# Kernel tuning notes

Measured on AMD Instinct MI355X. Metric: run time of the kernel, lower is better.

The kernel has to match this reference:

```python
import jax, jax.numpy as jnp
import numpy as np

N = 131072   # n_nodes == n_edges (required by the broadcast in the original module)
C = 256      # node_channels == edge_channels (required by the broadcast)
EPS_BN = 1e-5
EPS = 1e-5


def _linear_params(key, out_c, in_c):
    k1, k2 = jax.random.split(key)
    bound = 1.0 / np.sqrt(in_c)
    W = jax.random.uniform(k1, (out_c, in_c), minval=-bound, maxval=bound, dtype=jnp.float32)
    b = jax.random.uniform(k2, (out_c,), minval=-bound, maxval=bound, dtype=jnp.float32)
    return W, b


def setup_inputs() -> dict:
    key = jax.random.key(0)
    ks = jax.random.split(key, 10)
    h = jax.random.normal(ks[0], (N, C), dtype=jnp.float32)
    e = jax.random.normal(ks[1], (N, C), dtype=jnp.float32)
    edge_index = jax.random.randint(ks[2], (2, N), 0, N, dtype=jnp.int64)
    A_w, A_b = _linear_params(ks[3], C, C)
    B_w, B_b = _linear_params(ks[4], C, C)
    C_w, C_b = _linear_params(ks[5], C, C)
    D_w, D_b = _linear_params(ks[6], C, C)
    U_w, U_b = _linear_params(ks[7], C, C)
    V_w, V_b = _linear_params(ks[8], C, C)
    bn_gamma = jnp.ones((C,), dtype=jnp.float32)
    bn_beta = jnp.zeros((C,), dtype=jnp.float32)
    return dict(h=h, edge_index=edge_index, e=e,
                A_w=A_w, A_b=A_b, B_w=B_w, B_b=B_b,
                C_w=C_w, C_b=C_b, D_w=D_w, D_b=D_b,
                bn_gamma=bn_gamma, bn_beta=bn_beta,
                U_w=U_w, U_b=U_b, V_w=V_w, V_b=V_b)


def reference(h, edge_index, e,
              A_w, A_b, B_w, B_b, C_w, C_b, D_w, D_b,
              bn_gamma, bn_beta, U_w, U_b, V_w, V_b):
    row, col = edge_index[0], edge_index[1]
    # gather + four parallel linears, summed: [E, C]
    e_out = (h[row] @ A_w.T + A_b
             + h[col] @ B_w.T + B_b
             + e[col] @ C_w.T + C_b
             + e[row] @ D_w.T + D_b)
    # BatchNorm1d (training mode: batch stats, biased variance) + ReLU
    mu = jnp.mean(e_out, axis=0)
    var = jnp.var(e_out, axis=0)
    e_out = jax.nn.relu(bn_gamma * (e_out - mu) * jax.lax.rsqrt(var + EPS_BN) + bn_beta)
    # scatter-add edge messages into node-indexed e, then sigmoid-normalize over dim 0
    e_new = e.at[row].add(e_out)
    e_new = jax.nn.sigmoid(e_new)
    e_new = e_new / (jnp.sum(e_new, axis=0, keepdims=True) + EPS)
    # final gather-multiply-reduce: (e_new * V(h[col])).sum(0) broadcasts [N,C]*[E,C] with N==E
    h_out = h @ U_w.T + U_b + jnp.sum(e_new * (h[col] @ V_w.T + V_b), axis=0)
    h_out = jax.nn.relu(h_out)
    return h_out, e_new
```

## Files before the change

kernel.cpp:

```cpp
#include <hip/hip_runtime.h>
#include <hip/hip_bf16.h>


typedef __attribute__((ext_vector_type(8))) short bf16x8;
typedef __attribute__((ext_vector_type(4))) float f32x4;

__device__ __forceinline__ float b2f(unsigned int lo16) {
  union { unsigned int u; float f; } c; c.u = lo16 << 16; return c.f;
}
__device__ __forceinline__ float lof(unsigned int u) { return b2f(u & 0xffffu); }
__device__ __forceinline__ float hif(unsigned int u) { return b2f(u >> 16); }
__device__ __forceinline__ unsigned int f2b(float f) {
  union { float f; unsigned int u; } c; c.f = f;
  unsigned int u = c.u;
  u += 0x7fffu + ((u >> 16) & 1u);
  return u >> 16;
}

__device__ __forceinline__ void prep_chunk(const float* __restrict__ src,
                                           unsigned short* __restrict__ dst, int g) {
  int mtile = g >> 9;
  int rem = g & 511;
  int r = rem >> 5, k8 = rem & 31;
  const float4* s = reinterpret_cast<const float4*>(src + (((size_t)mtile * 16 + r) << 8) + k8 * 8);
  float4 v0 = s[0], v1 = s[1];
  uint4 o;
  o.x = f2b(v0.x) | (f2b(v0.y) << 16);
  o.y = f2b(v0.z) | (f2b(v0.w) << 16);
  o.z = f2b(v1.x) | (f2b(v1.y) << 16);
  o.w = f2b(v1.z) | (f2b(v1.w) << 16);
  *reinterpret_cast<uint4*>(dst + ((size_t)mtile * 512 + k8 * 16 + r) * 8) = o;
}

__global__ __launch_bounds__(256) void prep_he(const float* __restrict__ h,
                                               unsigned short* __restrict__ h_t,
                                               const float* __restrict__ e,
                                               unsigned short* __restrict__ e_t,
                                               int nChunksEach) {
  int g = blockIdx.x * 256 + threadIdx.x;
  if (g < nChunksEach) prep_chunk(h, h_t, g);
  else if (g < 2 * nChunksEach) prep_chunk(e, e_t, g - nChunksEach);
}

__global__ __launch_bounds__(256) void prep_weights(
    const float* __restrict__ s0, const float* __restrict__ s1,
    const float* __restrict__ s2, const float* __restrict__ s3,
    const float* __restrict__ s4, const float* __restrict__ s5,
    unsigned short* __restrict__ W1h, unsigned short* __restrict__ W1e,
    unsigned short* __restrict__ W2t,
    const float* __restrict__ Ab, const float* __restrict__ Db,
    const float* __restrict__ Bb, const float* __restrict__ Cb,
    const float* __restrict__ Vb, const float* __restrict__ Ub,
    float* __restrict__ b1, float* __restrict__ b2,
    float* __restrict__ sums, float* __restrict__ sumsq,
    float* __restrict__ colsum, float* __restrict__ Traw,
    const int* __restrict__ ei, int* __restrict__ mode) {
  int g = blockIdx.x * 256 + threadIdx.x;
  if (blockIdx.x == 0) {
    const int t = threadIdx.x;
    b1[t] = Ab[t] + Db[t];
    b1[256 + t] = Bb[t] + Cb[t];
    b2[t] = Vb[t];
    b2[256 + t] = Ub[t];
    sums[t] = 0.f; sumsq[t] = 0.f; colsum[t] = 0.f; Traw[t] = 0.f;
    if (t == 0) {
      int m = 0;
#pragma unroll
      for (int i = 1; i < 64; i += 2) m |= ei[i];
      *mode = (m == 0) ? 1 : 0;
    }
  }
  int sel = g >> 13;
  int gg = g & 8191;
  const float* src; unsigned short* dst;
  switch (sel) {
    case 0: src = s0; dst = W1h; break;
    case 1: src = s1; dst = W1h + 65536; break;
    case 2: src = s2; dst = W1e; break;
    case 3: src = s3; dst = W1e + 65536; break;
    case 4: src = s4; dst = W2t; break;
    default: src = s5; dst = W2t + 65536; break;
  }
  prep_chunk(src, dst, gg);
}

__global__ __launch_bounds__(256) void gemm_bt2(
    const unsigned short* __restrict__ Ah, const unsigned short* __restrict__ Ae,
    const unsigned short* __restrict__ Bh, const unsigned short* __restrict__ Be,
    const float* __restrict__ bias, unsigned short* __restrict__ Cmat,
    int O, int nColBlk, int ktSteps, int nBlk) {
  __shared__ char lds[49152];
  const int cpx = nBlk >> 3;
  const int hw = blockIdx.x;
  const int bid = (hw % 8) * cpx + hw / 8;
  const int colBlk = bid % nColBlk;
  const int rowBlk = bid / nColBlk;
  const int tid = threadIdx.x;
  const int w = tid >> 6, lane = tid & 63;
  const int wm = w >> 1, wn = w & 1;

  const size_t aTileOff = (size_t)(rowBlk * 8 + w * 2) * 8192 + lane * 16;
  const size_t bTileOff = (size_t)(colBlk * 8 + w * 2) * 8192 + lane * 16;
  const int wOff0 = (w * 2) * 1024;
  const int wOff1 = (w * 2 + 1) * 1024;

  f32x4 acc[4][4] = {};

  auto stage = [&](int kt, char* bufA, char* bufB) {
    const char* Ab_ = (const char*)(kt < 8 ? Ah : Ae) + aTileOff + (size_t)(kt & 7) * 1024;
    const char* Bb_ = (const char*)(kt < 8 ? Bh : Be) + bTileOff + (size_t)(kt & 7) * 1024;
    __builtin_amdgcn_global_load_lds((const __attribute__((address_space(1))) void*)Ab_,
                                     (__attribute__((address_space(3))) void*)(bufA + wOff0), 16, 0, 0);
    __builtin_amdgcn_global_load_lds((const __attribute__((address_space(1))) void*)(Ab_ + 8192),
                                     (__attribute__((address_space(3))) void*)(bufA + wOff1), 16, 0, 0);
    __builtin_amdgcn_global_load_lds((const __attribute__((address_space(1))) void*)Bb_,
                                     (__attribute__((address_space(3))) void*)(bufB + wOff0), 16, 0, 0);
    __builtin_amdgcn_global_load_lds((const __attribute__((address_space(1))) void*)(Bb_ + 8192),
                                     (__attribute__((address_space(3))) void*)(bufB + wOff1), 16, 0, 0);
  };
  auto computeFrom = [&](const char* bufA, const char* bufB) {
    bf16x8 a[4], b[4];
#pragma unroll
    for (int mi = 0; mi < 4; ++mi)
      a[mi] = *reinterpret_cast<const bf16x8*>(bufA + (wm * 4 + mi) * 1024 + lane * 16);
#pragma unroll
    for (int ni = 0; ni < 4; ++ni)
      b[ni] = *reinterpret_cast<const bf16x8*>(bufB + (wn * 4 + ni) * 1024 + lane * 16);
#pragma unroll
    for (int mi = 0; mi < 4; ++mi)
#pragma unroll
      for (int ni = 0; ni < 4; ++ni)
        acc[mi][ni] = __builtin_amdgcn_mfma_f32_16x16x32_bf16(a[mi], b[ni], acc[mi][ni], 0, 0, 0);
  };

  char* A0 = lds;          char* A1 = lds + 8192;   char* A2 = lds + 16384;
  char* B0 = lds + 24576;  char* B1 = lds + 32768;  char* B2 = lds + 40960;

  stage(0, A0, B0);
  stage(1, A1, B1);
  char *Ac = A0, *An = A1, *Aq = A2;
  char *Bc = B0, *Bn = B1, *Bq = B2;

#pragma unroll 1
  for (int kt = 0; kt < ktSteps; ++kt) {
    if (kt + 1 < ktSteps) {
      asm volatile("s_waitcnt vmcnt(4)" ::: "memory");
    } else {
      asm volatile("s_waitcnt vmcnt(0)" ::: "memory");
    }
    __builtin_amdgcn_s_barrier();
    asm volatile("" ::: "memory");
    __builtin_amdgcn_sched_barrier(0);
    if (kt + 2 < ktSteps) stage(kt + 2, Aq, Bq);
    computeFrom(Ac, Bc);
    char* tA = Ac; Ac = An; An = Aq; Aq = tA;
    char* tB = Bc; Bc = Bn; Bn = Bq; Bq = tB;
  }

  const int rb = rowBlk * 128 + wm * 64 + ((lane >> 4) << 2);
  const int cb = colBlk * 128 + wn * 64 + (lane & 15);
#pragma unroll
  for (int mi = 0; mi < 4; ++mi) {
#pragma unroll
    for (int ni = 0; ni < 4; ++ni) {
      const int coln = cb + ni * 16;
      const float bz = bias[coln];
      const size_t base = (size_t)(rb + mi * 16) * O + coln;
#pragma unroll
      for (int r = 0; r < 4; ++r)
        Cmat[base + (size_t)r * O] = (unsigned short)f2b(acc[mi][ni][r] + bz);
    }
  }
}

__global__ __launch_bounds__(256) void edge_stats(
    const unsigned short* __restrict__ PRPC,
    const int* __restrict__ rows_s, const int* __restrict__ cols_s,
    float* __restrict__ sums, float* __restrict__ sumsq) {
  __shared__ float red[8][256];
  const int c8 = threadIdx.x & 31;
  const int sub = threadIdx.x >> 5;
  float s[8], q[8];
#pragma unroll
  for (int j = 0; j < 8; ++j) { s[j] = 0.f; q[j] = 0.f; }
#pragma unroll 1
  for (int grp = 0; grp < 2; ++grp) {
    const int kb = blockIdx.x * 64 + grp * 32 + sub * 4;
    int r[4], cj[4];
#pragma unroll
    for (int u = 0; u < 4; ++u) { r[u] = rows_s[kb + u]; cj[u] = cols_s[kb + u]; }
    uint4 pr[4], pc[4];
#pragma unroll
    for (int u = 0; u < 4; ++u)
      pr[u] = *reinterpret_cast<const uint4*>(PRPC + (size_t)r[u] * 512 + c8 * 8);
#pragma unroll
    for (int u = 0; u < 4; ++u)
      pc[u] = *reinterpret_cast<const uint4*>(PRPC + (size_t)cj[u] * 512 + 256 + c8 * 8);
#pragma unroll
    for (int u = 0; u < 4; ++u) {
      const unsigned int rw[4] = {pr[u].x, pr[u].y, pr[u].z, pr[u].w};
      const unsigned int cw[4] = {pc[u].x, pc[u].y, pc[u].z, pc[u].w};
#pragma unroll
      for (int p4 = 0; p4 < 4; ++p4) {
        const float v0 = lof(rw[p4]) + lof(cw[p4]);
        const float v1 = hif(rw[p4]) + hif(cw[p4]);
        s[2 * p4] += v0;     q[2 * p4] += v0 * v0;
        s[2 * p4 + 1] += v1; q[2 * p4 + 1] += v1 * v1;
      }
    }
  }
#pragma unroll
  for (int j = 0; j < 8; ++j) red[sub][c8 * 8 + j] = s[j];
  __syncthreads();
  {
    const int c = threadIdx.x;
    float t = 0.f;
#pragma unroll
    for (int u2 = 0; u2 < 8; ++u2) t += red[u2][c];
    atomicAdd(sums + c, t);
  }
  __syncthreads();
#pragma unroll
  for (int j = 0; j < 8; ++j) red[sub][c8 * 8 + j] = q[j];
  __syncthreads();
  {
    const int c = threadIdx.x;
    float t = 0.f;
#pragma unroll
    for (int u2 = 0; u2 < 8; ++u2) t += red[u2][c];
    atomicAdd(sumsq + c, t);
  }
}

__global__ __launch_bounds__(256) void hist_rows(const int* __restrict__ ei,
                                                 const int* __restrict__ modep,
                                                 int* __restrict__ cnt, int Nn) {
  const int k = blockIdx.x * 256 + threadIdx.x;
  if (k >= Nn) return;
  const int row = (*modep) ? ei[2 * k] : ei[k];
  atomicAdd(&cnt[row], 1);
}

__global__ __launch_bounds__(256) void scan1(const int* __restrict__ cnt,
                                             int* __restrict__ bsum) {
  __shared__ int red[256];
  const int t = threadIdx.x;
  red[t] = cnt[blockIdx.x * 256 + t];
  __syncthreads();
#pragma unroll
  for (int s = 128; s > 0; s >>= 1) {
    if (t < s) red[t] += red[t + s];
    __syncthreads();
  }
  if (t == 0) bsum[blockIdx.x] = red[0];
}

__global__ __launch_bounds__(512) void scan2(int* __restrict__ bsum, int nb) {
  __shared__ int tmp[512];
  const int t = threadIdx.x;
  const int own = (t < nb) ? bsum[t] : 0;
  tmp[t] = own;
  __syncthreads();
  for (int off = 1; off < 512; off <<= 1) {
    int v = (t >= off) ? tmp[t - off] : 0;
    __syncthreads();
    tmp[t] += v;
    __syncthreads();
  }
  if (t < nb) bsum[t] = tmp[t] - own;
}

__global__ __launch_bounds__(256) void scan3(const int* __restrict__ cnt,
                                             const int* __restrict__ bsum,
                                             int* __restrict__ base, int Nn) {
  __shared__ int tmp[256];
  const int t = threadIdx.x;
  const int gid = blockIdx.x * 256 + t;
  const int own = cnt[gid];
  tmp[t] = own;
  __syncthreads();
  for (int off = 1; off < 256; off <<= 1) {
    int v = (t >= off) ? tmp[t - off] : 0;
    __syncthreads();
    tmp[t] += v;
    __syncthreads();
  }
  base[gid] = tmp[t] - own + bsum[blockIdx.x];
  if (gid == 0) base[Nn] = Nn;
}

__global__ __launch_bounds__(256) void scatter_eids(const int* __restrict__ ei,
                                                    const int* __restrict__ modep,
                                                    const int* __restrict__ base,
                                                    int* __restrict__ cnt,
                                                    int* __restrict__ rows_s,
                                                    int* __restrict__ cols_s, int Nn) {
  const int k = blockIdx.x * 256 + threadIdx.x;
  if (k >= Nn) return;
  int row, col;
  if (*modep) { row = ei[2 * k]; col = ei[2 * (Nn + k)]; }
  else        { row = ei[k];     col = ei[Nn + k]; }
  const int pos = base[row] + atomicAdd(&cnt[row], -1) - 1;
  rows_s[pos] = row;
  cols_s[pos] = col;
}

#define GCAP 1024
__global__ __launch_bounds__(256) void gather_sig_T(
    const float* __restrict__ e, const unsigned short* __restrict__ PRPC,
    const int* __restrict__ base, const int* __restrict__ cols_s,
    const int* __restrict__ ei, const int* __restrict__ modep,
    const unsigned short* __restrict__ VU,
    const float* __restrict__ sums, const float* __restrict__ sumsq,
    const float* __restrict__ gamma, const float* __restrict__ beta,
    unsigned short* __restrict__ accB, float* __restrict__ colsum,
    float* __restrict__ Traw, float invE, int Nn) {
  __shared__ float red[4][256];
  __shared__ int colsL[GCAP];
  __shared__ int baseL[65];
  const int lane = threadIdx.x & 63, w = threadIdx.x >> 6;
  const int n0 = blockIdx.x * 64;
  if (threadIdx.x < 65) baseL[threadIdx.x] = base[n0 + threadIdx.x];
  __syncthreads();
  const int bstart = baseL[0];
  const int bcount = baseL[64] - bstart;
  for (int qq = threadIdx.x; qq < bcount && qq < GCAP; qq += 256)
    colsL[qq] = cols_s[bstart + qq];
  const float4 sm = *reinterpret_cast<const float4*>(sums + lane * 4);
  const float4 sq = *reinterpret_cast<const float4*>(sumsq + lane * 4);
  const float4 gm = *reinterpret_cast<const float4*>(gamma + lane * 4);
  const float4 bt = *reinterpret_cast<const float4*>(beta + lane * 4);
  float4 sc, sh;
  {
    const float mx = sm.x * invE, my = sm.y * invE, mz = sm.z * invE, mw = sm.w * invE;
    sc.x = gm.x * rsqrtf(fmaxf(sq.x * invE - mx * mx, 0.f) + 1e-5f);
    sc.y = gm.y * rsqrtf(fmaxf(sq.y * invE - my * my, 0.f) + 1e-5f);
    sc.z = gm.z * rsqrtf(fmaxf(sq.z * invE - mz * mz, 0.f) + 1e-5f);
    sc.w = gm.w * rsqrtf(fmaxf(sq.w * invE - mw * mw, 0.f) + 1e-5f);
    sh.x = bt.x - mx * sc.x; sh.y = bt.y - my * sc.y;
    sh.z = bt.z - mz * sc.z; sh.w = bt.w - mw * sc.w;
  }
  __syncthreads();
  const int mode = *modep;
  float s0 = 0.f, s1 = 0.f, s2 = 0.f, s3 = 0.f;
  float t0 = 0.f, t1 = 0.f, t2 = 0.f, t3 = 0.f;
  const int i0 = n0 + w * 16;
  int p = baseL[w * 16];
  const int pendW = baseL[w * 16 + 16];
  uint2 pcn; pcn.x = 0; pcn.y = 0;
  if (p < pendW) {
    const int q0 = p - bstart;
    const int cj = (q0 < GCAP) ? colsL[q0] : cols_s[p];
    pcn = *reinterpret_cast<const uint2*>(PRPC + (size_t)cj * 512 + 256 + lane * 4);
  }
  float4 ev = *reinterpret_cast<const float4*>(e + (size_t)i0 * 256 + lane * 4);
  uint2 prv = *reinterpret_cast<const uint2*>(PRPC + (size_t)i0 * 512 + lane * 4);
#pragma unroll 1
  for (int it = 0; it < 16; ++it) {
    const int i = i0 + it;
    const int colT = mode ? ei[2 * (Nn + i)] : ei[Nn + i];
    const uint2 hv = *reinterpret_cast<const uint2*>(VU + (size_t)colT * 512 + lane * 4);
    float4 v = ev;
    const uint2 pr = prv;
    if (it + 1 < 16) {
      ev = *reinterpret_cast<const float4*>(e + (size_t)(i + 1) * 256 + lane * 4);
      prv = *reinterpret_cast<const uint2*>(PRPC + (size_t)(i + 1) * 512 + lane * 4);
    }
    const float pr0 = lof(pr.x), pr1 = hif(pr.x), pr2 = lof(pr.y), pr3 = hif(pr.y);
    const int pe = baseL[w * 16 + it + 1];
#pragma unroll 1
    while (p < pe) {
      const uint2 pc = pcn;
      if (p + 1 < pendW) {
        const int qn = p + 1 - bstart;
        const int cj = (qn < GCAP) ? colsL[qn] : cols_s[p + 1];
        pcn = *reinterpret_cast<const uint2*>(PRPC + (size_t)cj * 512 + 256 + lane * 4);
      }
      v.x += fmaxf(fmaf(sc.x, pr0 + lof(pc.x), sh.x), 0.f);
      v.y += fmaxf(fmaf(sc.y, pr1 + hif(pc.x), sh.y), 0.f);
      v.z += fmaxf(fmaf(sc.z, pr2 + lof(pc.y), sh.z), 0.f);
      v.w += fmaxf(fmaf(sc.w, pr3 + hif(pc.y), sh.w), 0.f);
      ++p;
    }
    v.x = 1.f / (1.f + __expf(-v.x));
    v.y = 1.f / (1.f + __expf(-v.y));
    v.z = 1.f / (1.f + __expf(-v.z));
    v.w = 1.f / (1.f + __expf(-v.w));
    uint2 ob;
    ob.x = f2b(v.x) | (f2b(v.y) << 16);
    ob.y = f2b(v.z) | (f2b(v.w) << 16);
    *reinterpret_cast<uint2*>(accB + (size_t)i * 256 + lane * 4) = ob;
    s0 += v.x; s1 += v.y; s2 += v.z; s3 += v.w;
    t0 += v.x * lof(hv.x); t1 += v.y * hif(hv.x);
    t2 += v.z * lof(hv.y); t3 += v.w * hif(hv.y);
  }
  red[w][lane * 4 + 0] = s0;
  red[w][lane * 4 + 1] = s1;
  red[w][lane * 4 + 2] = s2;
  red[w][lane * 4 + 3] = s3;
  __syncthreads();
  {
    const int c = threadIdx.x;
    atomicAdd(colsum + c, red[0][c] + red[1][c] + red[2][c] + red[3][c]);
  }
  __syncthreads();
  red[w][lane * 4 + 0] = t0;
  red[w][lane * 4 + 1] = t1;
  red[w][lane * 4 + 2] = t2;
  red[w][lane * 4 + 3] = t3;
  __syncthreads();
  {
    const int c = threadIdx.x;
    atomicAdd(Traw + c, red[0][c] + red[1][c] + red[2][c] + red[3][c]);
  }
}

__global__ __launch_bounds__(256) void finalize(
    const unsigned short* __restrict__ accB, const unsigned short* __restrict__ VU,
    const float* __restrict__ colsum, const float* __restrict__ Traw,
    float* __restrict__ outE, float* __restrict__ outH, int nChunks) {
  const int g = blockIdx.x * 256 + threadIdx.x;
  if (g >= nChunks) return;
  const int i = g >> 5, c8 = g & 31;
  const float4 cs0 = *reinterpret_cast<const float4*>(colsum + c8 * 8);
  const float4 cs1 = *reinterpret_cast<const float4*>(colsum + c8 * 8 + 4);
  const float4 tr0 = *reinterpret_cast<const float4*>(Traw + c8 * 8);
  const float4 tr1 = *reinterpret_cast<const float4*>(Traw + c8 * 8 + 4);
  float iv[8] = {1.f / (cs0.x + 1e-5f), 1.f / (cs0.y + 1e-5f),
                 1.f / (cs0.z + 1e-5f), 1.f / (cs0.w + 1e-5f),
                 1.f / (cs1.x + 1e-5f), 1.f / (cs1.y + 1e-5f),
                 1.f / (cs1.z + 1e-5f), 1.f / (cs1.w + 1e-5f)};
  float tt[8] = {tr0.x * iv[0], tr0.y * iv[1], tr0.z * iv[2], tr0.w * iv[3],
                 tr1.x * iv[4], tr1.y * iv[5], tr1.z * iv[6], tr1.w * iv[7]};
  const uint4 sb = *reinterpret_cast<const uint4*>(accB + (size_t)i * 256 + c8 * 8);
  const unsigned int sw[4] = {sb.x, sb.y, sb.z, sb.w};
  float4 e0, e1;
  e0.x = lof(sw[0]) * iv[0]; e0.y = hif(sw[0]) * iv[1];
  e0.z = lof(sw[1]) * iv[2]; e0.w = hif(sw[1]) * iv[3];
  e1.x = lof(sw[2]) * iv[4]; e1.y = hif(sw[2]) * iv[5];
  e1.z = lof(sw[3]) * iv[6]; e1.w = hif(sw[3]) * iv[7];
  float4* qe = reinterpret_cast<float4*>(outE + (size_t)i * 256 + c8 * 8);
  qe[0] = e0; qe[1] = e1;
  const uint4 hu = *reinterpret_cast<const uint4*>(VU + (size_t)i * 512 + 256 + c8 * 8);
  float4 o0, o1;
  o0.x = fmaxf(lof(hu.x) + tt[0], 0.f);
  o0.y = fmaxf(hif(hu.x) + tt[1], 0.f);
  o0.z = fmaxf(lof(hu.y) + tt[2], 0.f);
  o0.w = fmaxf(hif(hu.y) + tt[3], 0.f);
  o1.x = fmaxf(lof(hu.z) + tt[4], 0.f);
  o1.y = fmaxf(hif(hu.z) + tt[5], 0.f);
  o1.z = fmaxf(lof(hu.w) + tt[6], 0.f);
  o1.w = fmaxf(hif(hu.w) + tt[7], 0.f);
  float4* qh = reinterpret_cast<float4*>(outH + (size_t)i * 256 + c8 * 8);
  qh[0] = o0; qh[1] = o1;
}

extern "C" void kernel_launch(void* const* d_in, const int* in_sizes, int n_in,
                              void* d_out, int out_size, void* d_ws, size_t ws_size,
                              hipStream_t stream) {
  const float* h     = (const float*)d_in[0];
  const int*   ei    = (const int*)d_in[1];
  const float* e     = (const float*)d_in[2];
  const float* Aw    = (const float*)d_in[3];
  const float* Ab    = (const float*)d_in[4];
  const float* Bw    = (const float*)d_in[5];
  const float* Bb    = (const float*)d_in[6];
  const float* Cw    = (const float*)d_in[7];
  const float* Cb    = (const float*)d_in[8];
  const float* Dw    = (const float*)d_in[9];
  const float* Db    = (const float*)d_in[10];
  const float* gamma = (const float*)d_in[11];
  const float* beta  = (const float*)d_in[12];
  const float* Uw    = (const float*)d_in[13];
  const float* Ub    = (const float*)d_in[14];
  const float* Vw    = (const float*)d_in[15];
  const float* Vb    = (const float*)d_in[16];
  const int N = in_sizes[0] / 256;

  char* ws = (char*)d_ws;
  unsigned short* W1h = (unsigned short*)(ws + 0x0);
  unsigned short* W1e = (unsigned short*)(ws + 0x40000);
  unsigned short* W2t = (unsigned short*)(ws + 0x80000);
  float* b1     = (float*)(ws + 0xC0000);
  float* b2     = (float*)(ws + 0xC0800);
  float* sums   = (float*)(ws + 0xC1000);
  float* sumsq  = (float*)(ws + 0xC1400);
  float* colsum = (float*)(ws + 0xC1800);
  float* Traw   = (float*)(ws + 0xC1C00);
  int*   mode   = (int*)(ws + 0xC2C00);
  unsigned short* h_t  = (unsigned short*)(ws + 0x100000);
  unsigned short* e_t  = (unsigned short*)(ws + 0x4100000);
  unsigned short* PRPC = (unsigned short*)(ws + 0x8100000);
  unsigned short* VU   = (unsigned short*)(ws + 0x10100000);
  unsigned short* accB = (unsigned short*)(ws + 0x100000);
  int* cnt    = (int*)(ws + 0x18100000);
  int* baseA  = (int*)(ws + 0x18180000);
  int* rows_s = (int*)(ws + 0x18210000);
  int* cols_s = (int*)(ws + 0x18290000);
  int* bsum   = (int*)(ws + 0x18310000);

  float* outH = (float*)d_out;
  float* outE = outH + (size_t)N * 256;

  hipMemsetAsync(cnt, 0, (size_t)N * 4, stream);
  prep_weights<<<192, 256, 0, stream>>>(Aw, Bw, Dw, Cw, Vw, Uw, W1h, W1e, W2t,
                                        Ab, Db, Bb, Cb, Vb, Ub, b1, b2,
                                        sums, sumsq, colsum, Traw, ei, mode);

  hist_rows<<<N / 256, 256, 0, stream>>>(ei, mode, cnt, N);
  scan1<<<N / 256, 256, 0, stream>>>(cnt, bsum);
  scan2<<<1, 512, 0, stream>>>(bsum, N / 256);
  scan3<<<N / 256, 256, 0, stream>>>(cnt, bsum, baseA, N);
  scatter_eids<<<N / 256, 256, 0, stream>>>(ei, mode, baseA, cnt, rows_s, cols_s, N);

  const int nChunks = N * 32;
  prep_he<<<2 * nChunks / 256, 256, 0, stream>>>(h, h_t, e, e_t, nChunks);
  gemm_bt2<<<(N / 128) * 4, 256, 0, stream>>>(h_t, e_t, W1h, W1e, b1, PRPC, 512, 4, 16, (N / 128) * 4);
  gemm_bt2<<<(N / 128) * 4, 256, 0, stream>>>(h_t, h_t, W2t, W2t, b2, VU, 512, 4, 8, (N / 128) * 4);

  edge_stats<<<N / 64, 256, 0, stream>>>(PRPC, rows_s, cols_s, sums, sumsq);
  gather_sig_T<<<N / 64, 256, 0, stream>>>(e, PRPC, baseA, cols_s, ei, mode, VU,
                                           sums, sumsq, gamma, beta,
                                           accB, colsum, Traw, 1.0f / (float)N, N);
  finalize<<<nChunks / 256, 256, 0, stream>>>(accB, VU, colsum, Traw, outE, outH, nChunks);
}
```

Before: 539.6 us.

## Merge the two GEMM launches and make edge_stats walk the CSR row segments

The two bf16 GEMM launches are combined into one grid: blocks index into either the first GEMM (h/e against W1) or the second (h against W2), which removes one launch and lets the tail of one GEMM overlap the other. edge_stats now walks the row-sorted CSR segments per node. It loads each row's PRPC slice once and prefetches the column gathers, so the rows_s array and its writes in scatter_eids are no longer needed. In exchange, the data-dependent while loops can leave waves unevenly loaded when node degrees are skewed, and each lane now handles 4 channels with 8-byte loads.

```diff
diff --git a/kernel.cpp b/kernel.cpp
--- a/kernel.cpp
+++ b/kernel.cpp
@@ -84,14 +84,26 @@
   prep_chunk(src, dst, gg);
 }
 
-__global__ __launch_bounds__(256) void gemm_bt2(
-    const unsigned short* __restrict__ Ah, const unsigned short* __restrict__ Ae,
-    const unsigned short* __restrict__ Bh, const unsigned short* __restrict__ Be,
-    const float* __restrict__ bias, unsigned short* __restrict__ Cmat,
-    int O, int nColBlk, int ktSteps, int nBlk) {
+__global__ __launch_bounds__(256) void gemm_fused(
+    const unsigned short* __restrict__ h_t, const unsigned short* __restrict__ e_t,
+    const unsigned short* __restrict__ W1h, const unsigned short* __restrict__ W1e,
+    const unsigned short* __restrict__ W2t,
+    const float* __restrict__ b1, const float* __restrict__ b2,
+    unsigned short* __restrict__ PRPC, unsigned short* __restrict__ VU,
+    int nB1) {
   __shared__ char lds[49152];
-  const int cpx = nBlk >> 3;
-  const int hw = blockIdx.x;
+  const int g = blockIdx.x;
+  const bool is2 = (g >= nB1);
+  const int hw = is2 ? (g - nB1) : g;
+  const unsigned short* Ah = h_t;
+  const unsigned short* Ae = e_t;
+  const unsigned short* Bh = is2 ? W2t : W1h;
+  const unsigned short* Be = is2 ? W2t : W1e;
+  const float* bias = is2 ? b2 : b1;
+  unsigned short* Cmat = is2 ? VU : PRPC;
+  const int ktSteps = is2 ? 8 : 16;
+  const int O = 512, nColBlk = 4;
+  const int cpx = nB1 >> 3;
   const int bid = (hw % 8) * cpx + hw / 8;
   const int colBlk = bid % nColBlk;
   const int rowBlk = bid / nColBlk;
@@ -173,65 +185,6 @@
   }
 }
 
-__global__ __launch_bounds__(256) void edge_stats(
-    const unsigned short* __restrict__ PRPC,
-    const int* __restrict__ rows_s, const int* __restrict__ cols_s,
-    float* __restrict__ sums, float* __restrict__ sumsq) {
-  __shared__ float red[8][256];
-  const int c8 = threadIdx.x & 31;
-  const int sub = threadIdx.x >> 5;
-  float s[8], q[8];
-#pragma unroll
-  for (int j = 0; j < 8; ++j) { s[j] = 0.f; q[j] = 0.f; }
-#pragma unroll 1
-  for (int grp = 0; grp < 2; ++grp) {
-    const int kb = blockIdx.x * 64 + grp * 32 + sub * 4;
-    int r[4], cj[4];
-#pragma unroll
-    for (int u = 0; u < 4; ++u) { r[u] = rows_s[kb + u]; cj[u] = cols_s[kb + u]; }
-    uint4 pr[4], pc[4];
-#pragma unroll
-    for (int u = 0; u < 4; ++u)
-      pr[u] = *reinterpret_cast<const uint4*>(PRPC + (size_t)r[u] * 512 + c8 * 8);
-#pragma unroll
-    for (int u = 0; u < 4; ++u)
-      pc[u] = *reinterpret_cast<const uint4*>(PRPC + (size_t)cj[u] * 512 + 256 + c8 * 8);
-#pragma unroll
-    for (int u = 0; u < 4; ++u) {
-      const unsigned int rw[4] = {pr[u].x, pr[u].y, pr[u].z, pr[u].w};
-      const unsigned int cw[4] = {pc[u].x, pc[u].y, pc[u].z, pc[u].w};
-#pragma unroll
-      for (int p4 = 0; p4 < 4; ++p4) {
-        const float v0 = lof(rw[p4]) + lof(cw[p4]);
-        const float v1 = hif(rw[p4]) + hif(cw[p4]);
-        s[2 * p4] += v0;     q[2 * p4] += v0 * v0;
-        s[2 * p4 + 1] += v1; q[2 * p4 + 1] += v1 * v1;
-      }
-    }
-  }
-#pragma unroll
-  for (int j = 0; j < 8; ++j) red[sub][c8 * 8 + j] = s[j];
-  __syncthreads();
-  {
-    const int c = threadIdx.x;
-    float t = 0.f;
-#pragma unroll
-    for (int u2 = 0; u2 < 8; ++u2) t += red[u2][c];
-    atomicAdd(sums + c, t);
-  }
-  __syncthreads();
-#pragma unroll
-  for (int j = 0; j < 8; ++j) red[sub][c8 * 8 + j] = q[j];
-  __syncthreads();
-  {
-    const int c = threadIdx.x;
-    float t = 0.f;
-#pragma unroll
-    for (int u2 = 0; u2 < 8; ++u2) t += red[u2][c];
-    atomicAdd(sumsq + c, t);
-  }
-}
-
 __global__ __launch_bounds__(256) void hist_rows(const int* __restrict__ ei,
                                                  const int* __restrict__ modep,
                                                  int* __restrict__ cnt, int Nn) {
@@ -293,7 +246,6 @@
                                                     const int* __restrict__ modep,
                                                     const int* __restrict__ base,
                                                     int* __restrict__ cnt,
-                                                    int* __restrict__ rows_s,
                                                     int* __restrict__ cols_s, int Nn) {
   const int k = blockIdx.x * 256 + threadIdx.x;
   if (k >= Nn) return;
@@ -301,11 +253,86 @@
   if (*modep) { row = ei[2 * k]; col = ei[2 * (Nn + k)]; }
   else        { row = ei[k];     col = ei[Nn + k]; }
   const int pos = base[row] + atomicAdd(&cnt[row], -1) - 1;
-  rows_s[pos] = row;
   cols_s[pos] = col;
 }
 
 #define GCAP 1024
+
+__global__ __launch_bounds__(256) void edge_stats(
+    const unsigned short* __restrict__ PRPC,
+    const int* __restrict__ base, const int* __restrict__ cols_s,
+    float* __restrict__ sums, float* __restrict__ sumsq) {
+  __shared__ float red[4][256];
+  __shared__ int colsL[GCAP];
+  __shared__ int baseL[65];
+  const int lane = threadIdx.x & 63, w = threadIdx.x >> 6;
+  const int n0 = blockIdx.x * 64;
+  if (threadIdx.x < 65) baseL[threadIdx.x] = base[n0 + threadIdx.x];
+  __syncthreads();
+  const int bstart = baseL[0];
+  const int bcount = baseL[64] - bstart;
+  for (int qq = threadIdx.x; qq < bcount && qq < GCAP; qq += 256)
+    colsL[qq] = cols_s[bstart + qq];
+  __syncthreads();
+  float s0 = 0.f, s1 = 0.f, s2 = 0.f, s3 = 0.f;
+  float q0 = 0.f, q1 = 0.f, q2 = 0.f, q3 = 0.f;
+  const int i0 = n0 + w * 16;
+  int p = baseL[w * 16];
+  const int pendW = baseL[w * 16 + 16];
+  uint2 pcn; pcn.x = 0; pcn.y = 0;
+  if (p < pendW) {
+    const int qq0 = p - bstart;
+    const int cj = (qq0 < GCAP) ? colsL[qq0] : cols_s[p];
+    pcn = *reinterpret_cast<const uint2*>(PRPC + (size_t)cj * 512 + 256 + lane * 4);
+  }
+  uint2 prv = *reinterpret_cast<const uint2*>(PRPC + (size_t)i0 * 512 + lane * 4);
+#pragma unroll 1
+  for (int it = 0; it < 16; ++it) {
+    const uint2 pr = prv;
+    if (it + 1 < 16)
+      prv = *reinterpret_cast<const uint2*>(PRPC + (size_t)(i0 + it + 1) * 512 + lane * 4);
+    const float pr0 = lof(pr.x), pr1 = hif(pr.x), pr2 = lof(pr.y), pr3 = hif(pr.y);
+    const int pe = baseL[w * 16 + it + 1];
+#pragma unroll 1
+    while (p < pe) {
+      const uint2 pc = pcn;
+      if (p + 1 < pendW) {
+        const int qn = p + 1 - bstart;
+        const int cj = (qn < GCAP) ? colsL[qn] : cols_s[p + 1];
+        pcn = *reinterpret_cast<const uint2*>(PRPC + (size_t)cj * 512 + 256 + lane * 4);
+      }
+      const float v0 = pr0 + lof(pc.x);
+      const float v1 = pr1 + hif(pc.x);
+      const float v2 = pr2 + lof(pc.y);
+      const float v3 = pr3 + hif(pc.y);
+      s0 += v0; q0 += v0 * v0;
+      s1 += v1; q1 += v1 * v1;
+      s2 += v2; q2 += v2 * v2;
+      s3 += v3; q3 += v3 * v3;
+      ++p;
+    }
+  }
+  red[w][lane * 4 + 0] = s0;
+  red[w][lane * 4 + 1] = s1;
+  red[w][lane * 4 + 2] = s2;
+  red[w][lane * 4 + 3] = s3;
+  __syncthreads();
+  {
+    const int c = threadIdx.x;
+    atomicAdd(sums + c, red[0][c] + red[1][c] + red[2][c] + red[3][c]);
+  }
+  __syncthreads();
+  red[w][lane * 4 + 0] = q0;
+  red[w][lane * 4 + 1] = q1;
+  red[w][lane * 4 + 2] = q2;
+  red[w][lane * 4 + 3] = q3;
+  __syncthreads();
+  {
+    const int c = threadIdx.x;
+    atomicAdd(sumsq + c, red[0][c] + red[1][c] + red[2][c] + red[3][c]);
+  }
+}
+
 __global__ __launch_bounds__(256) void gather_sig_T(
     const float* __restrict__ e, const unsigned short* __restrict__ PRPC,
     const int* __restrict__ base, const int* __restrict__ cols_s,
@@ -495,7 +522,6 @@
   unsigned short* accB = (unsigned short*)(ws + 0x100000);
   int* cnt    = (int*)(ws + 0x18100000);
   int* baseA  = (int*)(ws + 0x18180000);
-  int* rows_s = (int*)(ws + 0x18210000);
   int* cols_s = (int*)(ws + 0x18290000);
   int* bsum   = (int*)(ws + 0x18310000);
 
@@ -511,14 +537,14 @@
   scan1<<<N / 256, 256, 0, stream>>>(cnt, bsum);
   scan2<<<1, 512, 0, stream>>>(bsum, N / 256);
   scan3<<<N / 256, 256, 0, stream>>>(cnt, bsum, baseA, N);
-  scatter_eids<<<N / 256, 256, 0, stream>>>(ei, mode, baseA, cnt, rows_s, cols_s, N);
+  scatter_eids<<<N / 256, 256, 0, stream>>>(ei, mode, baseA, cnt, cols_s, N);
 
   const int nChunks = N * 32;
   prep_he<<<2 * nChunks / 256, 256, 0, stream>>>(h, h_t, e, e_t, nChunks);
-  gemm_bt2<<<(N / 128) * 4, 256, 0, stream>>>(h_t, e_t, W1h, W1e, b1, PRPC, 512, 4, 16, (N / 128) * 4);
-  gemm_bt2<<<(N / 128) * 4, 256, 0, stream>>>(h_t, h_t, W2t, W2t, b2, VU, 512, 4, 8, (N / 128) * 4);
-
-  edge_stats<<<N / 64, 256, 0, stream>>>(PRPC, rows_s, cols_s, sums, sumsq);
+  const int nB1 = (N / 128) * 4;
+  gemm_fused<<<2 * nB1, 256, 0, stream>>>(h_t, e_t, W1h, W1e, W2t, b1, b2, PRPC, VU, nB1);
+
+  edge_stats<<<N / 64, 256, 0, stream>>>(PRPC, baseA, cols_s, sums, sumsq);
   gather_sig_T<<<N / 64, 256, 0, stream>>>(e, PRPC, baseA, cols_s, ei, mode, VU,
                                            sums, sumsq, gamma, beta,
                                            accB, colsum, Traw, 1.0f / (float)N, N);
```

New measurement: 554.7 us. 1.03x slower.

## Load GEMM B fragments straight to registers and halve LDS staging

Applied to the files above, without the earlier changes.

The gemm_bt2 kernel no longer stages the B (weight) operand through LDS. Each wave now loads its B fragments directly from global memory into registers, double-buffered across an unrolled-by-two k loop, while A keeps its triple-buffered global_load_lds path. LDS per block drops from 48KB to 24KB, which can raise occupancy and cuts LDS reads for B. In exchange, waves sharing a column block issue duplicate B global loads. The hand-written vmcnt waits also become more delicate to keep correct.

```diff
diff --git a/kernel.cpp b/kernel.cpp
--- a/kernel.cpp
+++ b/kernel.cpp
@@ -89,7 +89,7 @@
     const unsigned short* __restrict__ Bh, const unsigned short* __restrict__ Be,
     const float* __restrict__ bias, unsigned short* __restrict__ Cmat,
     int O, int nColBlk, int ktSteps, int nBlk) {
-  __shared__ char lds[49152];
+  __shared__ char lds[24576];
   const int cpx = nBlk >> 3;
   const int hw = blockIdx.x;
   const int bid = (hw % 8) * cpx + hw / 8;
@@ -100,32 +100,31 @@
   const int wm = w >> 1, wn = w & 1;
 
   const size_t aTileOff = (size_t)(rowBlk * 8 + w * 2) * 8192 + lane * 16;
-  const size_t bTileOff = (size_t)(colBlk * 8 + w * 2) * 8192 + lane * 16;
+  const size_t bFragOff = (size_t)(colBlk * 8 + wn * 4) * 8192 + lane * 16;
   const int wOff0 = (w * 2) * 1024;
   const int wOff1 = (w * 2 + 1) * 1024;
 
   f32x4 acc[4][4] = {};
-
-  auto stage = [&](int kt, char* bufA, char* bufB) {
+  bf16x8 b0[4], b1v[4];
+
+  auto stageA = [&](int kt, char* buf) {
     const char* Ab_ = (const char*)(kt < 8 ? Ah : Ae) + aTileOff + (size_t)(kt & 7) * 1024;
-    const char* Bb_ = (const char*)(kt < 8 ? Bh : Be) + bTileOff + (size_t)(kt & 7) * 1024;
     __builtin_amdgcn_global_load_lds((const __attribute__((address_space(1))) void*)Ab_,
-                                     (__attribute__((address_space(3))) void*)(bufA + wOff0), 16, 0, 0);
+                                     (__attribute__((address_space(3))) void*)(buf + wOff0), 16, 0, 0);
     __builtin_amdgcn_global_load_lds((const __attribute__((address_space(1))) void*)(Ab_ + 8192),
-                                     (__attribute__((address_space(3))) void*)(bufA + wOff1), 16, 0, 0);
-    __builtin_amdgcn_global_load_lds((const __attribute__((address_space(1))) void*)Bb_,
-                                     (__attribute__((address_space(3))) void*)(bufB + wOff0), 16, 0, 0);
-    __builtin_amdgcn_global_load_lds((const __attribute__((address_space(1))) void*)(Bb_ + 8192),
-                                     (__attribute__((address_space(3))) void*)(bufB + wOff1), 16, 0, 0);
+                                     (__attribute__((address_space(3))) void*)(buf + wOff1), 16, 0, 0);
   };
-  auto computeFrom = [&](const char* bufA, const char* bufB) {
-    bf16x8 a[4], b[4];
+  auto loadB = [&](int kt, bf16x8* dst) {
+    const char* p = (const char*)(kt < 8 ? Bh : Be) + bFragOff + (size_t)(kt & 7) * 1024;
+#pragma unroll
+    for (int ni = 0; ni < 4; ++ni)
+      dst[ni] = *reinterpret_cast<const bf16x8*>(p + (size_t)ni * 8192);
+  };
+  auto computeFrom = [&](const char* bufA, const bf16x8* b) {
+    bf16x8 a[4];
 #pragma unroll
     for (int mi = 0; mi < 4; ++mi)
       a[mi] = *reinterpret_cast<const bf16x8*>(bufA + (wm * 4 + mi) * 1024 + lane * 16);
-#pragma unroll
-    for (int ni = 0; ni < 4; ++ni)
-      b[ni] = *reinterpret_cast<const bf16x8*>(bufB + (wn * 4 + ni) * 1024 + lane * 16);
 #pragma unroll
     for (int mi = 0; mi < 4; ++mi)
 #pragma unroll
@@ -133,28 +132,35 @@
         acc[mi][ni] = __builtin_amdgcn_mfma_f32_16x16x32_bf16(a[mi], b[ni], acc[mi][ni], 0, 0, 0);
   };
 
-  char* A0 = lds;          char* A1 = lds + 8192;   char* A2 = lds + 16384;
-  char* B0 = lds + 24576;  char* B1 = lds + 32768;  char* B2 = lds + 40960;
-
-  stage(0, A0, B0);
-  stage(1, A1, B1);
+  char* A0 = lds; char* A1 = lds + 8192; char* A2 = lds + 16384;
+
+  loadB(0, b0);
+  stageA(0, A0);
+  stageA(1, A1);
   char *Ac = A0, *An = A1, *Aq = A2;
-  char *Bc = B0, *Bn = B1, *Bq = B2;
 
 #pragma unroll 1
-  for (int kt = 0; kt < ktSteps; ++kt) {
-    if (kt + 1 < ktSteps) {
-      asm volatile("s_waitcnt vmcnt(4)" ::: "memory");
-    } else {
-      asm volatile("s_waitcnt vmcnt(0)" ::: "memory");
-    }
+  for (int kt = 0; kt < ktSteps; kt += 2) {
+    if (kt < ktSteps - 1) { asm volatile("s_waitcnt vmcnt(2)" ::: "memory"); }
+    else                  { asm volatile("s_waitcnt vmcnt(0)" ::: "memory"); }
     __builtin_amdgcn_s_barrier();
     asm volatile("" ::: "memory");
     __builtin_amdgcn_sched_barrier(0);
-    if (kt + 2 < ktSteps) stage(kt + 2, Aq, Bq);
-    computeFrom(Ac, Bc);
-    char* tA = Ac; Ac = An; An = Aq; Aq = tA;
-    char* tB = Bc; Bc = Bn; Bn = Bq; Bq = tB;
+    if (kt + 1 < ktSteps) loadB(kt + 1, b1v);
+    if (kt + 2 < ktSteps) stageA(kt + 2, Aq);
+    computeFrom(Ac, b0);
+    { char* t = Ac; Ac = An; An = Aq; Aq = t; }
+    if (kt + 1 < ktSteps) {
+      if (kt + 2 < ktSteps) { asm volatile("s_waitcnt vmcnt(2)" ::: "memory"); }
+      else                  { asm volatile("s_waitcnt vmcnt(0)" ::: "memory"); }
+      __builtin_amdgcn_s_barrier();
+      asm volatile("" ::: "memory");
+      __builtin_amdgcn_sched_barrier(0);
+      if (kt + 2 < ktSteps) loadB(kt + 2, b0);
+      if (kt + 3 < ktSteps) stageA(kt + 3, Aq);
+      computeFrom(Ac, b1v);
+      { char* t = Ac; Ac = An; An = Aq; Aq = t; }
+    }
   }
 
   const int rb = rowBlk * 128 + wm * 64 + ((lane >> 4) << 2);
```

Result: slower. 580.3 us (+7.6%).
